# Kernel tuning notes

Measured on AMD Instinct MI355X. Metric: run time of the kernel, lower is better.

The kernel has to match this reference:

```python
import jax, jax.numpy as jnp
import numpy as np

S, B, C = 7, 2, 20
LAMBDA_COORD = 5.0
LAMBDA_NOOBJ = 0.5
EPS_WH = 1e-6
EPS_IOU = 1e-6
BATCH = 16384


def _iou_yolo(b1, b2):
    # b*: [..., 4] in (xc, yc, w, h) format
    b1x1 = b1[..., 0] - b1[..., 2] / 2
    b1y1 = b1[..., 1] - b1[..., 3] / 2
    b1x2 = b1[..., 0] + b1[..., 2] / 2
    b1y2 = b1[..., 1] + b1[..., 3] / 2
    b2x1 = b2[..., 0] - b2[..., 2] / 2
    b2y1 = b2[..., 1] - b2[..., 3] / 2
    b2x2 = b2[..., 0] + b2[..., 2] / 2
    b2y2 = b2[..., 1] + b2[..., 3] / 2
    iw = jnp.clip(jnp.minimum(b1x2, b2x2) - jnp.maximum(b1x1, b2x1), 0.0)
    ih = jnp.clip(jnp.minimum(b1y2, b2y2) - jnp.maximum(b1y1, b2y1), 0.0)
    inter = iw * ih
    a1 = jnp.abs((b1x2 - b1x1) * (b1y2 - b1y1))
    a2 = jnp.abs((b2x2 - b2x1) * (b2y2 - b2y1))
    return inter / (a1 + a2 - inter + EPS_IOU)


def setup_inputs() -> dict:
    key = jax.random.key(0)
    k1, k2, k3 = jax.random.split(key, 3)
    y_trues = jax.random.uniform(k1, (BATCH, S, S, 5 * B + C), dtype=jnp.float32)
    # conf1 channel must be exactly 1.0 for object cells (code checks == 1)
    obj = (jax.random.uniform(k3, (BATCH, S, S)) < 0.3).astype(jnp.float32)
    y_trues = y_trues.at[..., 4].set(obj)
    y_preds = jax.random.normal(k2, (BATCH, S, S, 5 * B + C), dtype=jnp.float32)
    return {"y_trues": y_trues, "y_preds": y_preds}


def reference(y_trues, y_preds):
    bs = y_trues.shape[0]
    yt = y_trues.reshape(bs, S * S, C + B * 5)
    yp = y_preds.reshape(bs, S * S, C + B * 5)

    obj = (yt[..., 4] == 1.0)            # [bs, S*S] bool
    objf = obj.astype(yt.dtype)
    noobjf = 1.0 - objf

    b = yt[..., 0:4]
    bhat1 = yp[..., 0:4]
    bhat2 = yp[..., 5:9]

    iou1 = _iou_yolo(b, bhat1)
    iou2 = _iou_yolo(b, bhat2)
    best1 = iou1 > iou2                  # [bs, S*S]

    bhat = jnp.where(best1[..., None], bhat1, bhat2)          # responsible box
    confhat = jnp.where(best1, yp[..., 4], yp[..., 9])

    # xy offset loss
    xy = (b[..., 0] - bhat[..., 0]) ** 2 + (b[..., 1] - bhat[..., 1]) ** 2
    xy_loss = LAMBDA_COORD * jnp.sum(objf * xy)

    # wh loss (sqrt targets, abs+eps on predictions)
    w_term = (jnp.sqrt(b[..., 2]) - jnp.sqrt(jnp.abs(bhat[..., 2] + EPS_WH))) ** 2
    h_term = (jnp.sqrt(b[..., 3]) - jnp.sqrt(jnp.abs(bhat[..., 3] + EPS_WH))) ** 2
    wh_loss = LAMBDA_COORD * jnp.sum(objf * (w_term + h_term))

    # object confidence loss (conf_i is 1 for obj cells)
    conf_loss = jnp.sum(objf * (yt[..., 4] - confhat) ** 2)

    # no-object confidence loss over both predicted boxes
    noobj_terms = (yt[..., 4:5] - yp[..., 4::5]) ** 2        # [bs, S*S, B]
    noobj_loss = LAMBDA_NOOBJ * jnp.sum(noobjf[..., None] * noobj_terms)

    # class loss
    cls = jnp.sum((yt[..., 10:] - yp[..., 10:]) ** 2, axis=-1)
    cls_loss = jnp.sum(objf * cls)

    total = xy_loss + wh_loss + conf_loss + noobj_loss + cls_loss
    return total / bs
```

## Files before the change

kernel.cpp:

```cpp
#include <hip/hip_runtime.h>

constexpr int   BATCH        = 16384;
constexpr int   CELLS        = 802816;
constexpr int   F            = 30;
constexpr int   CPB          = 128;
constexpr int   NTILES       = CELLS / CPB;
constexpr int   FLTS         = CPB * F;
constexpr int   TILE_B       = FLTS * 4;
constexpr int   CHUNK        = 1024;
constexpr int   NCHUNK       = TILE_B / CHUNK;
constexpr int   GRID         = 512;
constexpr float LAMBDA_COORD = 5.0f;
constexpr float LAMBDA_NOOBJ = 0.5f;
constexpr float EPS_WH       = 1e-6f;
constexpr float EPS_IOU      = 1e-6f;

__device__ __forceinline__ void load_lds16(const void* g, void* l) {
    __builtin_amdgcn_global_load_lds(
        (const __attribute__((address_space(1))) unsigned int*)g,
        (__attribute__((address_space(3))) unsigned int*)l,
        16, 0, 0);
}

__device__ __forceinline__ void block_barrier() {
    asm volatile("" ::: "memory");
    __builtin_amdgcn_s_barrier();
    asm volatile("" ::: "memory");
}

__device__ __forceinline__ float iou_yolo(const float b0, const float b1,
                                          const float b2, const float b3,
                                          const float c0, const float c1,
                                          const float c2, const float c3) {
    float b1x1 = b0 - b2 * 0.5f;
    float b1y1 = b1 - b3 * 0.5f;
    float b1x2 = b0 + b2 * 0.5f;
    float b1y2 = b1 + b3 * 0.5f;
    float b2x1 = c0 - c2 * 0.5f;
    float b2y1 = c1 - c3 * 0.5f;
    float b2x2 = c0 + c2 * 0.5f;
    float b2y2 = c1 + c3 * 0.5f;
    float iw = fmaxf(fminf(b1x2, b2x2) - fmaxf(b1x1, b2x1), 0.0f);
    float ih = fmaxf(fminf(b1y2, b2y2) - fmaxf(b1y1, b2y1), 0.0f);
    float inter = iw * ih;
    float a1 = fabsf((b1x2 - b1x1) * (b1y2 - b1y1));
    float a2 = fabsf((b2x2 - b2x1) * (b2y2 - b2y1));
    return inter / (a1 + a2 - inter + EPS_IOU);
}

__global__ void __launch_bounds__(128)
yolo_loss_kernel(const float* __restrict__ yt_g,
                 const float* __restrict__ yp_g,
                 float* __restrict__ out) {
    __shared__ __align__(16) float lbuf[2][2][FLTS];

    const int tid  = threadIdx.x;
    const int lane = tid & 63;
    const int wid  = tid >> 6;

    const char* src_base = (wid == 0) ? (const char*)yt_g : (const char*)yp_g;

    int tile = blockIdx.x;
    {
        const char* s = src_base + (size_t)tile * TILE_B + lane * 16;
        char* d = (char*)lbuf[0][wid];
#pragma unroll
        for (int j = 0; j < NCHUNK; ++j)
            load_lds16(s + j * CHUNK, d + j * CHUNK);
    }

    float acc = 0.0f;
    int buf = 0;

    for (; tile < NTILES; tile += GRID) {
        const int next = tile + GRID;
        if (next < NTILES) {
            const char* s = src_base + (size_t)next * TILE_B + lane * 16;
            char* d = (char*)lbuf[buf ^ 1][wid];
#pragma unroll
            for (int j = 0; j < NCHUNK; ++j)
                load_lds16(s + j * CHUNK, d + j * CHUNK);
            asm volatile("s_waitcnt vmcnt(15)" ::: "memory");
        } else {
            asm volatile("s_waitcnt vmcnt(0)" ::: "memory");
        }
        block_barrier();

        const float2* t2 = reinterpret_cast<const float2*>(&lbuf[buf][0][tid * F]);
        const float2* p2 = reinterpret_cast<const float2*>(&lbuf[buf][1][tid * F]);
        float t[F], p[F];
        {
            float2 v;
            v = t2[0]; t[0] = v.x; t[1] = v.y;
            v = t2[1]; t[2] = v.x; t[3] = v.y;
            v = t2[2]; t[4] = v.x;
#pragma unroll
            for (int k = 5; k < 15; ++k) { v = t2[k]; t[2 * k] = v.x; t[2 * k + 1] = v.y; }
        }
#pragma unroll
        for (int k = 0; k < 15; ++k) { float2 w = p2[k]; p[2 * k] = w.x; p[2 * k + 1] = w.y; }

        const float objf   = (t[4] == 1.0f) ? 1.0f : 0.0f;
        const float noobjf = 1.0f - objf;

        const float iou1 = iou_yolo(t[0], t[1], t[2], t[3], p[0], p[1], p[2], p[3]);
        const float iou2 = iou_yolo(t[0], t[1], t[2], t[3], p[5], p[6], p[7], p[8]);
        const bool  best1 = iou1 > iou2;

        const float bh0 = best1 ? p[0] : p[5];
        const float bh1 = best1 ? p[1] : p[6];
        const float bh2 = best1 ? p[2] : p[7];
        const float bh3 = best1 ? p[3] : p[8];
        const float confhat = best1 ? p[4] : p[9];

        const float dx = t[0] - bh0;
        const float dy = t[1] - bh1;
        const float xy = dx * dx + dy * dy;

        const float wt = sqrtf(t[2]) - sqrtf(fabsf(bh2 + EPS_WH));
        const float ht = sqrtf(t[3]) - sqrtf(fabsf(bh3 + EPS_WH));
        const float wh = wt * wt + ht * ht;

        const float dc = t[4] - confhat;

        float cls = 0.0f;
#pragma unroll
        for (int c = 10; c < F; ++c) {
            const float d = t[c] - p[c];
            cls += d * d;
        }
        float noobj = 0.0f;
#pragma unroll
        for (int c = 4; c < F; c += 5) {
            const float d = t[4] - p[c];
            noobj += d * d;
        }

        acc += objf * (LAMBDA_COORD * (xy + wh) + dc * dc + cls)
             + noobjf * (LAMBDA_NOOBJ * noobj);

        block_barrier();
        buf ^= 1;
    }

#pragma unroll
    for (int off = 32; off > 0; off >>= 1) acc += __shfl_down(acc, off);

    __shared__ float wsum[2];
    if (lane == 0) wsum[wid] = acc;
    __syncthreads();
    if (tid == 0) atomicAdd(out, (wsum[0] + wsum[1]) * (1.0f / (float)BATCH));
}

extern "C" void kernel_launch(void* const* d_in, const int* in_sizes, int n_in,
                              void* d_out, int out_size, void* d_ws, size_t ws_size,
                              hipStream_t stream) {
    const float* y_trues = (const float*)d_in[0];
    const float* y_preds = (const float*)d_in[1];
    float* out = (float*)d_out;

    hipMemsetAsync(out, 0, sizeof(float) * (size_t)out_size, stream);

    yolo_loss_kernel<<<GRID, 128, 0, stream>>>(y_trues, y_preds, out);
}
```

Measured before the change: 41.61 us.

## Use single-wave blocks with 64-cell tiles to drop block barriers

Each block becomes a single 64-thread wave that stages both the true and predicted tiles into LDS itself. Because no other wave shares the buffers, the per-iteration block barriers and the cross-wave reduction go away. The tile shrinks to 64 cells and the grid grows to 1280 blocks to add parallelism. The tile no longer splits evenly into 1 KB chunks, so a 4-byte LDS load tail is added, and the vmcnt wait count is retuned to match the new number of loads in flight.

```diff
diff --git a/kernel.cpp b/kernel.cpp
--- a/kernel.cpp
+++ b/kernel.cpp
@@ -3,13 +3,10 @@
 constexpr int   BATCH        = 16384;
 constexpr int   CELLS        = 802816;
 constexpr int   F            = 30;
-constexpr int   CPB          = 128;
-constexpr int   NTILES       = CELLS / CPB;
-constexpr int   FLTS         = CPB * F;
-constexpr int   TILE_B       = FLTS * 4;
-constexpr int   CHUNK        = 1024;
-constexpr int   NCHUNK       = TILE_B / CHUNK;
-constexpr int   GRID         = 512;
+constexpr int   CPT          = 64;
+constexpr int   NTILES       = CELLS / CPT;
+constexpr int   TILE_B       = CPT * F * 4;
+constexpr int   GRID         = 1280;
 constexpr float LAMBDA_COORD = 5.0f;
 constexpr float LAMBDA_NOOBJ = 0.5f;
 constexpr float EPS_WH       = 1e-6f;
@@ -21,11 +18,25 @@
         (__attribute__((address_space(3))) unsigned int*)l,
         16, 0, 0);
 }
+__device__ __forceinline__ void load_lds4(const void* g, void* l) {
+    __builtin_amdgcn_global_load_lds(
+        (const __attribute__((address_space(1))) unsigned int*)g,
+        (__attribute__((address_space(3))) unsigned int*)l,
+        4, 0, 0);
+}
 
-__device__ __forceinline__ void block_barrier() {
-    asm volatile("" ::: "memory");
-    __builtin_amdgcn_s_barrier();
-    asm volatile("" ::: "memory");
+__device__ __forceinline__ void stage_tile(const char* tg, const char* pg,
+                                           char* lt, char* lp, int lane) {
+#pragma unroll
+    for (int j = 0; j < 7; ++j) {
+        load_lds16(tg + j * 1024 + lane * 16, lt + j * 1024);
+        load_lds16(pg + j * 1024 + lane * 16, lp + j * 1024);
+    }
+#pragma unroll
+    for (int j = 0; j < 2; ++j) {
+        load_lds4(tg + 7168 + j * 256 + lane * 4, lt + 7168 + j * 256);
+        load_lds4(pg + 7168 + j * 256 + lane * 4, lp + 7168 + j * 256);
+    }
 }
 
 __device__ __forceinline__ float iou_yolo(const float b0, const float b1,
@@ -48,26 +59,18 @@
     return inter / (a1 + a2 - inter + EPS_IOU);
 }
 
-__global__ void __launch_bounds__(128)
+__global__ void __launch_bounds__(64)
 yolo_loss_kernel(const float* __restrict__ yt_g,
                  const float* __restrict__ yp_g,
                  float* __restrict__ out) {
-    __shared__ __align__(16) float lbuf[2][2][FLTS];
+    __shared__ __align__(16) float lbuf[2][2][CPT * F];
 
-    const int tid  = threadIdx.x;
-    const int lane = tid & 63;
-    const int wid  = tid >> 6;
-
-    const char* src_base = (wid == 0) ? (const char*)yt_g : (const char*)yp_g;
+    const int lane = threadIdx.x;
 
     int tile = blockIdx.x;
-    {
-        const char* s = src_base + (size_t)tile * TILE_B + lane * 16;
-        char* d = (char*)lbuf[0][wid];
-#pragma unroll
-        for (int j = 0; j < NCHUNK; ++j)
-            load_lds16(s + j * CHUNK, d + j * CHUNK);
-    }
+    stage_tile((const char*)yt_g + (size_t)tile * TILE_B,
+               (const char*)yp_g + (size_t)tile * TILE_B,
+               (char*)lbuf[0][0], (char*)lbuf[0][1], lane);
 
     float acc = 0.0f;
     int buf = 0;
@@ -75,19 +78,16 @@
     for (; tile < NTILES; tile += GRID) {
         const int next = tile + GRID;
         if (next < NTILES) {
-            const char* s = src_base + (size_t)next * TILE_B + lane * 16;
-            char* d = (char*)lbuf[buf ^ 1][wid];
-#pragma unroll
-            for (int j = 0; j < NCHUNK; ++j)
-                load_lds16(s + j * CHUNK, d + j * CHUNK);
-            asm volatile("s_waitcnt vmcnt(15)" ::: "memory");
+            stage_tile((const char*)yt_g + (size_t)next * TILE_B,
+                       (const char*)yp_g + (size_t)next * TILE_B,
+                       (char*)lbuf[buf ^ 1][0], (char*)lbuf[buf ^ 1][1], lane);
+            asm volatile("s_waitcnt vmcnt(18)" ::: "memory");
         } else {
             asm volatile("s_waitcnt vmcnt(0)" ::: "memory");
         }
-        block_barrier();
 
-        const float2* t2 = reinterpret_cast<const float2*>(&lbuf[buf][0][tid * F]);
-        const float2* p2 = reinterpret_cast<const float2*>(&lbuf[buf][1][tid * F]);
+        const float2* t2 = reinterpret_cast<const float2*>(&lbuf[buf][0][lane * F]);
+        const float2* p2 = reinterpret_cast<const float2*>(&lbuf[buf][1][lane * F]);
         float t[F], p[F];
         {
             float2 v;
@@ -139,17 +139,12 @@
         acc += objf * (LAMBDA_COORD * (xy + wh) + dc * dc + cls)
              + noobjf * (LAMBDA_NOOBJ * noobj);
 
-        block_barrier();
         buf ^= 1;
     }
 
 #pragma unroll
     for (int off = 32; off > 0; off >>= 1) acc += __shfl_down(acc, off);
-
-    __shared__ float wsum[2];
-    if (lane == 0) wsum[wid] = acc;
-    __syncthreads();
-    if (tid == 0) atomicAdd(out, (wsum[0] + wsum[1]) * (1.0f / (float)BATCH));
+    if (lane == 0) atomicAdd(out, acc * (1.0f / (float)BATCH));
 }
 
 extern "C" void kernel_launch(void* const* d_in, const int* in_sizes, int n_in,
@@ -161,5 +156,5 @@
 
     hipMemsetAsync(out, 0, sizeof(float) * (size_t)out_size, stream);
 
-    yolo_loss_kernel<<<GRID, 128, 0, stream>>>(y_trues, y_preds, out);
+    yolo_loss_kernel<<<GRID, 64, 0, stream>>>(y_trues, y_preds, out);
 }
```

Result: slower. 48.69 us (+17.0%).
